# Optimization experiments

Measured on AMD Instinct MI355X. Metric: run time of the kernel, lower is better.

## Reference

```python
import jax, jax.numpy as jnp
import numpy as np

BLOCK_SIZE = 512
EPS = 1e-06


def setup_inputs() -> dict:
    key = jax.random.key(0)
    k1, k2, k3 = jax.random.split(key, 3)
    B, H, S, D = 2, 32, 4096, 128
    return {
        "query_states": jax.random.normal(k1, (B, H, S, D), dtype=jnp.float32),
        "key_states": jax.random.normal(k2, (B, H, S, D), dtype=jnp.float32),
        "value_states": jax.random.normal(k3, (B, H, S, D), dtype=jnp.float32),
        "phi_scale": jnp.ones((H, 1, D), dtype=jnp.float32),
        "phi_bias": jnp.zeros((H, 1, D), dtype=jnp.float32),
    }


def _feature_map(x, phi_scale, phi_bias):
    # x: (B, H, N, S_blk, D); scale/bias: (H, 1, D) -> broadcast over (B, N)
    y = x * phi_scale[None, :, None] + phi_bias[None, :, None]
    return jax.nn.elu(y) + 1.0


def reference(query_states, key_states, value_states, phi_scale, phi_bias):
    B, H, S, D = query_states.shape
    nb = (S + BLOCK_SIZE - 1) // BLOCK_SIZE
    pad = nb * BLOCK_SIZE - S
    if pad > 0:
        p = [(0, 0), (0, 0), (0, pad), (0, 0)]
        query_states = jnp.pad(query_states, p)
        key_states = jnp.pad(key_states, p)
        value_states = jnp.pad(value_states, p)
    q = query_states.reshape(B, H, nb, BLOCK_SIZE, D)
    k = key_states.reshape(B, H, nb, BLOCK_SIZE, D)
    v = value_states.reshape(B, H, nb, BLOCK_SIZE, D)
    phi_q = _feature_map(q, phi_scale, phi_bias)
    phi_k = _feature_map(k, phi_scale, phi_bias)
    # per-block KV aggregation: S_dm = sum_s phi_k[s,d] v[s,m]
    S_dm = jnp.einsum('bhnsd,bhnsm->bhndm', phi_k, v)
    Z = phi_k.sum(axis=-2)  # (B, H, nb, D)
    num = jnp.einsum('bhnsd,bhndm->bhnsm', phi_q, S_dm)
    den = jnp.einsum('bhnsd,bhnd->bhns', phi_q, Z)[..., None] + EPS
    out = (num / den).reshape(B, H, nb * BLOCK_SIZE, D)
    if pad > 0:
        out = out[:, :, :S, :]
    return out
```

## Files before the change

### kernel.cpp

```cpp
#include <hip/hip_runtime.h>
#include <cstdint>

#define NH 32
#define SEQ 4096
#define DDIM 128
#define BSZ 512
#define SKC 64
#define NCH 8
#define KT_STRIDE 33
#define ST_STRIDE 68
#define OFF_KT 0
#define OFF_VT (128 * KT_STRIDE)
#define OFF_ST 0
#define OFF_QS (128 * ST_STRIDE)
#define OFF_Z  (OFF_QS + SKC * ST_STRIDE)
#define OFF_DEN (OFF_Z + 128)
#define LDS_DW (OFF_DEN + 64)

typedef _Float16 f16x8 __attribute__((ext_vector_type(8)));
typedef float f32x4 __attribute__((ext_vector_type(4)));

union FragU { uint32_t u[4]; f16x8 v; };

__device__ __forceinline__ float phi_fn(float x, float s, float b) {
    float y = fmaf(x, s, b);
    return y > 0.0f ? (y + 1.0f) : __expf(y);
}

__device__ __forceinline__ uint32_t pack_f16(float a, float b) {
    union { _Float16 h[2]; uint32_t u; } p;
    p.h[0] = (_Float16)a;
    p.h[1] = (_Float16)b;
    return p.u;
}

__global__ __launch_bounds__(256, 2) void linattn_kernel(
    const float* __restrict__ qg, const float* __restrict__ kg,
    const float* __restrict__ vg, const float* __restrict__ psg,
    const float* __restrict__ pbg, float* __restrict__ outg)
{
    __shared__ uint32_t lds[LDS_DW];
    float*    ldsf = (float*)lds;
    _Float16* ldsh = (_Float16*)lds;

    const int tid  = threadIdx.x;
    const int lane = tid & 63;
    const int wv   = tid >> 6;
    const int l15  = lane & 15;
    const int qd   = lane >> 4;

    const int gid = blockIdx.x;
    const int nb  = gid & 7;
    const int hh  = (gid >> 3) & 31;
    const int bb  = gid >> 8;

    const size_t base = ((size_t)(bb * NH + hh) * SEQ + (size_t)nb * BSZ) * DDIM;

    const int d1 = tid & 127;
    const int hf = tid >> 7;
    const float sc1 = psg[hh * DDIM + d1];
    const float bi1 = pbg[hh * DDIM + d1];

    const int d4 = (tid & 31) * 4;
    const float4 sc4 = *(const float4*)(psg + hh * DDIM + d4);
    const float4 bi4 = *(const float4*)(pbg + hh * DDIM + d4);

    if (tid < 128) ldsf[OFF_Z + tid] = 0.0f;

    float zacc = 0.0f;

    f32x4 acc[2][8];
    #pragma unroll
    for (int a = 0; a < 2; ++a)
        #pragma unroll
        for (int c = 0; c < 8; ++c)
            acc[a][c] = (f32x4){0.f, 0.f, 0.f, 0.f};

    for (int ch = 0; ch < NCH; ++ch) {
        __syncthreads();
        const float* kp = kg + base + (size_t)(ch * SKC) * DDIM + d1;
        const float* vp = vg + base + (size_t)(ch * SKC) * DDIM + d1;
        const int rowk = OFF_KT + d1 * KT_STRIDE + hf * 16;
        const int rowv = OFF_VT + d1 * KT_STRIDE + hf * 16;
        #pragma unroll 4
        for (int i = 0; i < 16; ++i) {
            const int sl = hf * 32 + 2 * i;
            float k0 = kp[(size_t)sl * DDIM];
            float k1 = kp[(size_t)(sl + 1) * DDIM];
            float v0 = vp[(size_t)sl * DDIM];
            float v1 = vp[(size_t)(sl + 1) * DDIM];
            float p0 = phi_fn(k0, sc1, bi1);
            float p1 = phi_fn(k1, sc1, bi1);
            zacc += p0 + p1;
            lds[rowk + i] = pack_f16(p0, p1);
            lds[rowv + i] = pack_f16(v0, v1);
        }
        __syncthreads();
        #pragma unroll
        for (int ks = 0; ks < 2; ++ks) {
            FragU af[2];
            #pragma unroll
            for (int tm = 0; tm < 2; ++tm) {
                const int m  = wv * 32 + tm * 16 + l15;
                const int ad = OFF_VT + m * KT_STRIDE + ks * 16 + qd * 4;
                af[tm].u[0] = lds[ad + 0]; af[tm].u[1] = lds[ad + 1];
                af[tm].u[2] = lds[ad + 2]; af[tm].u[3] = lds[ad + 3];
            }
            #pragma unroll
            for (int td = 0; td < 8; ++td) {
                const int dd = td * 16 + l15;
                const int bd = OFF_KT + dd * KT_STRIDE + ks * 16 + qd * 4;
                FragU bf;
                bf.u[0] = lds[bd + 0]; bf.u[1] = lds[bd + 1];
                bf.u[2] = lds[bd + 2]; bf.u[3] = lds[bd + 3];
                acc[0][td] = __builtin_amdgcn_mfma_f32_16x16x32_f16(af[0].v, bf.v, acc[0][td], 0, 0, 0);
                acc[1][td] = __builtin_amdgcn_mfma_f32_16x16x32_f16(af[1].v, bf.v, acc[1][td], 0, 0, 0);
            }
        }
    }

    atomicAdd(&ldsf[OFF_Z + d1], zacc);
    __syncthreads();

    #pragma unroll
    for (int tm = 0; tm < 2; ++tm)
        #pragma unroll
        for (int td = 0; td < 8; ++td)
            #pragma unroll
            for (int r = 0; r < 4; ++r) {
                const int m  = wv * 32 + tm * 16 + qd * 4 + r;
                const int dd = td * 16 + l15;
                ldsh[m * (ST_STRIDE * 2) + dd] = (_Float16)acc[tm][td][r];
            }

    const float4 zq = *(const float4*)(ldsf + OFF_Z + d4);

    const int sl2 = tid >> 5;
    for (int qc = 0; qc < 8; ++qc) {
        __syncthreads();
        const float* qp = qg + base + (size_t)(qc * SKC) * DDIM + d4;
        #pragma unroll 2
        for (int i = 0; i < 8; ++i) {
            const int srow = sl2 + i * 8;
            const float4 qv = *(const float4*)(qp + (size_t)srow * DDIM);
            float p0 = phi_fn(qv.x, sc4.x, bi4.x);
            float p1 = phi_fn(qv.y, sc4.y, bi4.y);
            float p2 = phi_fn(qv.z, sc4.z, bi4.z);
            float p3 = phi_fn(qv.w, sc4.w, bi4.w);
            const int ad = OFF_QS + srow * ST_STRIDE + (tid & 31) * 2;
            lds[ad + 0] = pack_f16(p0, p1);
            lds[ad + 1] = pack_f16(p2, p3);
            float pd = p0 * zq.x + p1 * zq.y + p2 * zq.z + p3 * zq.w;
            pd += __shfl_xor(pd, 16);
            pd += __shfl_xor(pd, 8);
            pd += __shfl_xor(pd, 4);
            pd += __shfl_xor(pd, 2);
            pd += __shfl_xor(pd, 1);
            if ((tid & 31) == 0) ldsf[OFF_DEN + srow] = pd;
        }
        __syncthreads();

        f32x4 acc2[8];
        #pragma unroll
        for (int c = 0; c < 8; ++c) acc2[c] = (f32x4){0.f, 0.f, 0.f, 0.f};

        #pragma unroll
        for (int ks = 0; ks < 4; ++ks) {
            const int srow = wv * 16 + l15;
            const int ad = OFF_QS + srow * ST_STRIDE + ks * 16 + qd * 4;
            FragU af;
            const uint4 t0 = *(const uint4*)(lds + ad);
            af.u[0] = t0.x; af.u[1] = t0.y; af.u[2] = t0.z; af.u[3] = t0.w;
            #pragma unroll
            for (int tn = 0; tn < 8; ++tn) {
                const int mm = tn * 16 + l15;
                const int bd = OFF_ST + mm * ST_STRIDE + ks * 16 + qd * 4;
                const uint4 t1 = *(const uint4*)(lds + bd);
                FragU bf;
                bf.u[0] = t1.x; bf.u[1] = t1.y; bf.u[2] = t1.z; bf.u[3] = t1.w;
                acc2[tn] = __builtin_amdgcn_mfma_f32_16x16x32_f16(af.v, bf.v, acc2[tn], 0, 0, 0);
            }
        }

        #pragma unroll
        for (int r = 0; r < 4; ++r) {
            const int srow = wv * 16 + qd * 4 + r;
            const float rden = 1.0f / (ldsf[OFF_DEN + srow] + 1e-6f);
            float* op = outg + base + (size_t)(qc * SKC + srow) * DDIM;
            #pragma unroll
            for (int tn = 0; tn < 8; ++tn)
                op[tn * 16 + l15] = acc2[tn][r] * rden;
        }
    }
}

extern "C" void kernel_launch(void* const* d_in, const int* in_sizes, int n_in,
                              void* d_out, int out_size, void* d_ws, size_t ws_size,
                              hipStream_t stream) {
    const float* q  = (const float*)d_in[0];
    const float* k  = (const float*)d_in[1];
    const float* v  = (const float*)d_in[2];
    const float* ps = (const float*)d_in[3];
    const float* pb = (const float*)d_in[4];
    float* out = (float*)d_out;
    linattn_kernel<<<dim3(512), dim3(256), 0, stream>>>(q, k, v, ps, pb, out);
}
```

Measured before the change: 431.7 us.

## Double-buffer K/V and Q staging with register prefetch two chunks ahead

```diff
diff --git a/kernel.cpp b/kernel.cpp
--- a/kernel.cpp
+++ b/kernel.cpp
@@ -9,13 +9,17 @@
 #define NCH 8
 #define KT_STRIDE 33
 #define ST_STRIDE 68
-#define OFF_KT 0
-#define OFF_VT (128 * KT_STRIDE)
+#define OFF_K0 0
+#define OFF_V0 (128 * KT_STRIDE)
+#define OFF_K1 (2 * 128 * KT_STRIDE)
+#define OFF_V1 (3 * 128 * KT_STRIDE)
 #define OFF_ST 0
-#define OFF_QS (128 * ST_STRIDE)
-#define OFF_Z  (OFF_QS + SKC * ST_STRIDE)
-#define OFF_DEN (OFF_Z + 128)
-#define LDS_DW (OFF_DEN + 64)
+#define OFF_QS0 (128 * ST_STRIDE)
+#define OFF_QS1 (OFF_QS0 + 64 * ST_STRIDE)
+#define OFF_Z   (OFF_QS1 + 64 * ST_STRIDE)
+#define OFF_DEN0 (OFF_Z + 128)
+#define OFF_DEN1 (OFF_DEN0 + 64)
+#define LDS_DW (OFF_DEN1 + 64)
 
 typedef _Float16 f16x8 __attribute__((ext_vector_type(8)));
 typedef float f32x4 __attribute__((ext_vector_type(4)));
@@ -56,18 +60,19 @@
 
     const size_t base = ((size_t)(bb * NH + hh) * SEQ + (size_t)nb * BSZ) * DDIM;
 
-    const int d1 = tid & 127;
-    const int hf = tid >> 7;
-    const float sc1 = psg[hh * DDIM + d1];
-    const float bi1 = pbg[hh * DDIM + d1];
-
-    const int d4 = (tid & 31) * 4;
+    const int dp = tid & 63;
+    const int qt = tid >> 6;
+    const float2 sc2 = *(const float2*)(psg + hh * DDIM + 2 * dp);
+    const float2 bi2 = *(const float2*)(pbg + hh * DDIM + 2 * dp);
+
+    const int d4  = (tid & 31) * 4;
+    const int sl2 = tid >> 5;
     const float4 sc4 = *(const float4*)(psg + hh * DDIM + d4);
     const float4 bi4 = *(const float4*)(pbg + hh * DDIM + d4);
 
     if (tid < 128) ldsf[OFF_Z + tid] = 0.0f;
 
-    float zacc = 0.0f;
+    float z0 = 0.0f, z1 = 0.0f;
 
     f32x4 acc[2][8];
     #pragma unroll
@@ -76,40 +81,54 @@
         for (int c = 0; c < 8; ++c)
             acc[a][c] = (f32x4){0.f, 0.f, 0.f, 0.f};
 
-    for (int ch = 0; ch < NCH; ++ch) {
-        __syncthreads();
-        const float* kp = kg + base + (size_t)(ch * SKC) * DDIM + d1;
-        const float* vp = vg + base + (size_t)(ch * SKC) * DDIM + d1;
-        const int rowk = OFF_KT + d1 * KT_STRIDE + hf * 16;
-        const int rowv = OFF_VT + d1 * KT_STRIDE + hf * 16;
-        #pragma unroll 4
-        for (int i = 0; i < 16; ++i) {
-            const int sl = hf * 32 + 2 * i;
-            float k0 = kp[(size_t)sl * DDIM];
-            float k1 = kp[(size_t)(sl + 1) * DDIM];
-            float v0 = vp[(size_t)sl * DDIM];
-            float v1 = vp[(size_t)(sl + 1) * DDIM];
-            float p0 = phi_fn(k0, sc1, bi1);
-            float p1 = phi_fn(k1, sc1, bi1);
-            zacc += p0 + p1;
-            lds[rowk + i] = pack_f16(p0, p1);
-            lds[rowv + i] = pack_f16(v0, v1);
-        }
-        __syncthreads();
+    float2 kr[16], vr[16];
+    const float* kbase = kg + base + 2 * dp;
+    const float* vbase = vg + base + 2 * dp;
+
+    auto loadkv = [&](int ch) {
+        const size_t off = (size_t)(ch * SKC + qt * 16) * DDIM;
+        #pragma unroll
+        for (int j = 0; j < 16; ++j) {
+            kr[j] = *(const float2*)(kbase + off + (size_t)j * DDIM);
+            vr[j] = *(const float2*)(vbase + off + (size_t)j * DDIM);
+        }
+    };
+    auto stagekv = [&](int buf) {
+        uint32_t* bk = lds + (buf ? OFF_K1 : OFF_K0) + qt * 8;
+        uint32_t* bv = lds + (buf ? OFF_V1 : OFF_V0) + qt * 8;
+        const int r0 = (2 * dp) * KT_STRIDE;
+        const int r1 = r0 + KT_STRIDE;
+        #pragma unroll
+        for (int j = 0; j < 8; ++j) {
+            float p0x = phi_fn(kr[2*j].x,   sc2.x, bi2.x);
+            float p1x = phi_fn(kr[2*j+1].x, sc2.x, bi2.x);
+            float p0y = phi_fn(kr[2*j].y,   sc2.y, bi2.y);
+            float p1y = phi_fn(kr[2*j+1].y, sc2.y, bi2.y);
+            z0 += p0x + p1x;
+            z1 += p0y + p1y;
+            bk[r0 + j] = pack_f16(p0x, p1x);
+            bk[r1 + j] = pack_f16(p0y, p1y);
+            bv[r0 + j] = pack_f16(vr[2*j].x, vr[2*j+1].x);
+            bv[r1 + j] = pack_f16(vr[2*j].y, vr[2*j+1].y);
+        }
+    };
+    auto mfma1 = [&](int buf) {
+        const int offK = buf ? OFF_K1 : OFF_K0;
+        const int offV = buf ? OFF_V1 : OFF_V0;
         #pragma unroll
         for (int ks = 0; ks < 2; ++ks) {
             FragU af[2];
             #pragma unroll
             for (int tm = 0; tm < 2; ++tm) {
                 const int m  = wv * 32 + tm * 16 + l15;
-                const int ad = OFF_VT + m * KT_STRIDE + ks * 16 + qd * 4;
+                const int ad = offV + m * KT_STRIDE + ks * 16 + qd * 4;
                 af[tm].u[0] = lds[ad + 0]; af[tm].u[1] = lds[ad + 1];
                 af[tm].u[2] = lds[ad + 2]; af[tm].u[3] = lds[ad + 3];
             }
             #pragma unroll
             for (int td = 0; td < 8; ++td) {
                 const int dd = td * 16 + l15;
-                const int bd = OFF_KT + dd * KT_STRIDE + ks * 16 + qd * 4;
+                const int bd = offK + dd * KT_STRIDE + ks * 16 + qd * 4;
                 FragU bf;
                 bf.u[0] = lds[bd + 0]; bf.u[1] = lds[bd + 1];
                 bf.u[2] = lds[bd + 2]; bf.u[3] = lds[bd + 3];
@@ -117,10 +136,21 @@
                 acc[1][td] = __builtin_amdgcn_mfma_f32_16x16x32_f16(af[1].v, bf.v, acc[1][td], 0, 0, 0);
             }
         }
+    };
+
+    loadkv(0);
+    stagekv(0);
+    loadkv(1);
+    __syncthreads();
+    for (int ch = 0; ch < NCH; ++ch) {
+        if (ch + 1 < NCH) stagekv((ch + 1) & 1);
+        if (ch + 2 < NCH) loadkv(ch + 2);
+        mfma1(ch & 1);
+        __syncthreads();
     }
 
-    atomicAdd(&ldsf[OFF_Z + d1], zacc);
-    __syncthreads();
+    atomicAdd(&ldsf[OFF_Z + 2 * dp],     z0);
+    atomicAdd(&ldsf[OFF_Z + 2 * dp + 1], z1);
 
     #pragma unroll
     for (int tm = 0; tm < 2; ++tm)
@@ -132,50 +162,70 @@
                 const int dd = td * 16 + l15;
                 ldsh[m * (ST_STRIDE * 2) + dd] = (_Float16)acc[tm][td][r];
             }
+    __syncthreads();
 
     const float4 zq = *(const float4*)(ldsf + OFF_Z + d4);
 
-    const int sl2 = tid >> 5;
-    for (int qc = 0; qc < 8; ++qc) {
-        __syncthreads();
-        const float* qp = qg + base + (size_t)(qc * SKC) * DDIM + d4;
-        #pragma unroll 2
+    float4 qr[8];
+    const float* qbase = qg + base + d4;
+
+    auto loadq = [&](int qc) {
+        const size_t off = (size_t)(qc * SKC) * DDIM;
+        #pragma unroll
+        for (int i = 0; i < 8; ++i)
+            qr[i] = *(const float4*)(qbase + off + (size_t)(sl2 + i * 8) * DDIM);
+    };
+    auto stageq = [&](int buf) {
+        uint32_t* qsb  = lds  + (buf ? OFF_QS1  : OFF_QS0);
+        float*    denb = ldsf + (buf ? OFF_DEN1 : OFF_DEN0);
+        #pragma unroll
         for (int i = 0; i < 8; ++i) {
             const int srow = sl2 + i * 8;
-            const float4 qv = *(const float4*)(qp + (size_t)srow * DDIM);
-            float p0 = phi_fn(qv.x, sc4.x, bi4.x);
-            float p1 = phi_fn(qv.y, sc4.y, bi4.y);
-            float p2 = phi_fn(qv.z, sc4.z, bi4.z);
-            float p3 = phi_fn(qv.w, sc4.w, bi4.w);
-            const int ad = OFF_QS + srow * ST_STRIDE + (tid & 31) * 2;
-            lds[ad + 0] = pack_f16(p0, p1);
-            lds[ad + 1] = pack_f16(p2, p3);
+            float p0 = phi_fn(qr[i].x, sc4.x, bi4.x);
+            float p1 = phi_fn(qr[i].y, sc4.y, bi4.y);
+            float p2 = phi_fn(qr[i].z, sc4.z, bi4.z);
+            float p3 = phi_fn(qr[i].w, sc4.w, bi4.w);
+            uint2 w;
+            w.x = pack_f16(p0, p1);
+            w.y = pack_f16(p2, p3);
+            *(uint2*)(qsb + srow * ST_STRIDE + (tid & 31) * 2) = w;
             float pd = p0 * zq.x + p1 * zq.y + p2 * zq.z + p3 * zq.w;
             pd += __shfl_xor(pd, 16);
             pd += __shfl_xor(pd, 8);
             pd += __shfl_xor(pd, 4);
             pd += __shfl_xor(pd, 2);
             pd += __shfl_xor(pd, 1);
-            if ((tid & 31) == 0) ldsf[OFF_DEN + srow] = pd;
-        }
-        __syncthreads();
+            if ((tid & 31) == 0) denb[srow] = pd;
+        }
+    };
+
+    loadq(0);
+    stageq(0);
+    loadq(1);
+    __syncthreads();
+
+    for (int qc = 0; qc < 8; ++qc) {
+        if (qc + 1 < 8) stageq((qc + 1) & 1);
+        if (qc + 2 < 8) loadq(qc + 2);
 
         f32x4 acc2[8];
         #pragma unroll
         for (int c = 0; c < 8; ++c) acc2[c] = (f32x4){0.f, 0.f, 0.f, 0.f};
+
+        const int qsOff  = (qc & 1) ? OFF_QS1  : OFF_QS0;
+        const int denOff = (qc & 1) ? OFF_DEN1 : OFF_DEN0;
 
         #pragma unroll
         for (int ks = 0; ks < 4; ++ks) {
             const int srow = wv * 16 + l15;
-            const int ad = OFF_QS + srow * ST_STRIDE + ks * 16 + qd * 4;
+            const int ad = qsOff + srow * ST_STRIDE + ks * 16 + qd * 4;
             FragU af;
             const uint4 t0 = *(const uint4*)(lds + ad);
             af.u[0] = t0.x; af.u[1] = t0.y; af.u[2] = t0.z; af.u[3] = t0.w;
             #pragma unroll
             for (int tn = 0; tn < 8; ++tn) {
                 const int mm = tn * 16 + l15;
-                const int bd = OFF_ST + mm * ST_STRIDE + ks * 16 + qd * 4;
-                const uint4 t1 = *(const uint4*)(lds + bd);
+                const uint4 t1 = *(const uint4*)(lds + OFF_ST + mm * ST_STRIDE + ks * 16 + qd * 4);
                 FragU bf;
                 bf.u[0] = t1.x; bf.u[1] = t1.y; bf.u[2] = t1.z; bf.u[3] = t1.w;
                 acc2[tn] = __builtin_amdgcn_mfma_f32_16x16x32_f16(af.v, bf.v, acc2[tn], 0, 0, 0);
@@ -185,12 +235,13 @@
         #pragma unroll
         for (int r = 0; r < 4; ++r) {
             const int srow = wv * 16 + qd * 4 + r;
-            const float rden = 1.0f / (ldsf[OFF_DEN + srow] + 1e-6f);
+            const float rden = 1.0f / (ldsf[denOff + srow] + 1e-6f);
             float* op = outg + base + (size_t)(qc * SKC + srow) * DDIM;
             #pragma unroll
             for (int tn = 0; tn < 8; ++tn)
-                op[tn * 16 + l15] = acc2[tn][r] * rden;
-        }
+                __builtin_nontemporal_store(acc2[tn][r] * rden, op + tn * 16 + l15);
+        }
+        if (qc + 1 < 8) __syncthreads();
     }
 }
 
```

Measured after the change: 405.4 us. -6.1%, faster.
